# Performance work log

Hardware: AMD Instinct MI355X
Metric: run time of the kernel (lower is better)

The kernel has to match this reference:

```python
import jax, jax.numpy as jnp
import numpy as np

EMBED_DIM = 64  # scale factor dim (matches head dim)


def setup_inputs() -> dict:
    key0 = jax.random.key(0)
    kq, kk, kv = jax.random.split(key0, 3)
    shape = (2, 16, 2048, 64)  # [B, H, S, D]
    return {
        "query": jax.random.normal(kq, shape, dtype=jnp.float32),
        "key": jax.random.normal(kk, shape, dtype=jnp.float32),
        "value": jax.random.normal(kv, shape, dtype=jnp.float32),
    }


def reference(query, key, value):
    # qk = Q K^T / sqrt(embed_dim); softmax over last dim; @ V
    inv_scale = jnp.sqrt(jnp.asarray(EMBED_DIM, dtype=query.dtype))
    scores = jnp.einsum("bhqd,bhkd->bhqk", query, key) / inv_scale
    probs = jax.nn.softmax(scores, axis=-1)
    # dropout_p=0.0 -> identity (eval semantics)
    return jnp.einsum("bhqk,bhkd->bhqd", probs, value)
```

## Files before the change

kernel.cpp:

```cpp
#include <hip/hip_runtime.h>
#include <hip/hip_bf16.h>

#define S_LEN 2048
#define DDIM  64
#define NT    (S_LEN / 64)
#define SCALE  0.125f
#define SCALE2 0.18033688f
#define NELEM  4194304
#define NQROW  65536
#define WC_LGKM0 0xc07f

#if __has_builtin(__builtin_amdgcn_permlane32_swap) && __has_builtin(__builtin_amdgcn_permlane16_swap)
#define HAVE_PLSWAP 1
#else
#define HAVE_PLSWAP 0
#endif

typedef __attribute__((ext_vector_type(8))) short short8;
typedef __attribute__((ext_vector_type(4))) float floatx4;

__device__ __forceinline__ short f2bf(float f) {
    union { float f; unsigned u; } v; v.f = f;
    return (short)((v.u + 0x7fffu + ((v.u >> 16) & 1u)) >> 16);
}

__device__ __forceinline__ unsigned pk2bf(float a, float b) {
    unsigned r;
    asm("v_cvt_pk_bf16_f32 %0, %1, %2" : "=v"(r) : "v"(a), "v"(b));
    return r;
}

__device__ __forceinline__ float fexp2(float x) {
#if __has_builtin(__builtin_amdgcn_exp2f)
    return __builtin_amdgcn_exp2f(x);
#else
    return exp2f(x);
#endif
}

#if HAVE_PLSWAP
__device__ __forceinline__ void plswap32(unsigned &a, unsigned &b) {
    auto r = __builtin_amdgcn_permlane32_swap((int)a, (int)b, false, false);
    a = (unsigned)r[0]; b = (unsigned)r[1];
}
__device__ __forceinline__ void plswap16(unsigned &a, unsigned &b) {
    auto r = __builtin_amdgcn_permlane16_swap((int)a, (int)b, false, false);
    a = (unsigned)r[0]; b = (unsigned)r[1];
}
#endif

__global__ __launch_bounds__(256) void prep_kv(const float* __restrict__ K,
                                               const float* __restrict__ V,
                                               short* __restrict__ Kb,
                                               short* __restrict__ Vt) {
    const int bh = blockIdx.x & 31;
    const int st = blockIdx.x >> 5;
    const int t  = threadIdx.x;
    const size_t tile_off = (size_t)bh * (S_LEN * DDIM) + (size_t)st * (64 * DDIM);

    {
        const float* src = K + tile_off + t * 16;
        short* dst = Kb + tile_off + t * 16;
        #pragma unroll
        for (int h = 0; h < 2; ++h) {
            float4 a = *(const float4*)(src + h * 8);
            float4 b = *(const float4*)(src + h * 8 + 4);
            uint4 o;
            o.x = pk2bf(a.x, a.y); o.y = pk2bf(a.z, a.w);
            o.z = pk2bf(b.x, b.y); o.w = pk2bf(b.z, b.w);
            *(uint4*)(dst + h * 8) = o;
        }
    }

    {
        const int s4 = (t & 15) * 4;
        const int d4 = (t >> 4) * 4;
        const float* src = V + tile_off;
        float4 v0 = *(const float4*)(src + (size_t)(s4 + 0) * 64 + d4);
        float4 v1 = *(const float4*)(src + (size_t)(s4 + 1) * 64 + d4);
        float4 v2 = *(const float4*)(src + (size_t)(s4 + 2) * 64 + d4);
        float4 v3 = *(const float4*)(src + (size_t)(s4 + 3) * 64 + d4);
        const float* r0 = (const float*)&v0;
        const float* r1 = (const float*)&v1;
        const float* r2 = (const float*)&v2;
        const float* r3 = (const float*)&v3;
        short* dstb = Vt + (size_t)bh * (DDIM * S_LEN) + (size_t)st * 64 + s4;
        #pragma unroll
        for (int dd = 0; dd < 4; ++dd) {
            uint2 o;
            o.x = pk2bf(r0[dd], r1[dd]);
            o.y = pk2bf(r2[dd], r3[dd]);
            *(uint2*)(dstb + (size_t)(d4 + dd) * S_LEN) = o;
        }
    }
}

__global__ __launch_bounds__(512) void attn_sm8(
    const float* __restrict__ Q, const short* __restrict__ Kb,
    const short* __restrict__ Vt, float* __restrict__ O)
{
    __shared__ short Ks[2][2][64 * 64];
    __shared__ short Vs[2][2][64 * 64];
    __shared__ float Dl[128];
#if !HAVE_PLSWAP
    __shared__ short Pl[8][32 * 64];
#endif

    constexpr int NIT = NT / 2;

    const int tid  = threadIdx.x;
    const int wave = tid >> 6;
    const int grp  = wave >> 2;
    const int w4   = wave & 3;
    const int lane = tid & 63;
    const int l16  = lane & 15;
    const int quad = lane >> 4;
    const int x7   = l16 & 7;

    const int bh = blockIdx.x & 31;
    const int qt = blockIdx.x >> 5;
    const int ks = grp;
    const size_t base = (size_t)bh * (S_LEN * DDIM);

    const int g   = tid & 255;
    const int ci0 = g,        r0 = ci0 >> 3, c0 = (ci0 & 7) ^ (r0 & 7);
    const int ci1 = 256 + g,  r1 = ci1 >> 3, c1 = (ci1 & 7) ^ (r1 & 7);
    const size_t koff = (size_t)ks * NIT * (64 * 64);
    const size_t voff = (size_t)ks * NIT * 64;
    const short* pK0 = Kb + base + koff + r0 * 64 + c0 * 8;
    const short* pK1 = Kb + base + koff + r1 * 64 + c1 * 8;
    const short* pV0 = Vt + base + voff + (size_t)r0 * S_LEN + c0 * 8;
    const short* pV1 = Vt + base + voff + (size_t)r1 * S_LEN + c1 * 8;

    short8 rk0 = *(const short8*)pK0;
    short8 rk1 = *(const short8*)pK1;
    short8 rv0 = *(const short8*)pV0;
    short8 rv1 = *(const short8*)pV1;

    short8 qf[2][2];
    #pragma unroll
    for (int nq = 0; nq < 2; ++nq) {
        const float* qp = Q + base + (size_t)(qt * 128 + w4 * 32 + nq * 16 + l16) * 64 + quad * 8;
        #pragma unroll
        for (int kt = 0; kt < 2; ++kt) {
            float4 a = *(const float4*)(qp + kt * 32);
            float4 b = *(const float4*)(qp + kt * 32 + 4);
            union { unsigned u[4]; short8 s; } qc;
            qc.u[0] = pk2bf(a.x * SCALE2, a.y * SCALE2);
            qc.u[1] = pk2bf(a.z * SCALE2, a.w * SCALE2);
            qc.u[2] = pk2bf(b.x * SCALE2, b.y * SCALE2);
            qc.u[3] = pk2bf(b.z * SCALE2, b.w * SCALE2);
            qf[nq][kt] = qc.s;
        }
    }

    floatx4 oacc[2][4];
    float rs[2];
    #pragma unroll
    for (int mt = 0; mt < 2; ++mt) {
        #pragma unroll
        for (int dt = 0; dt < 4; ++dt) oacc[mt][dt] = (floatx4){0.f,0.f,0.f,0.f};
        rs[mt] = 0.f;
    }

    short* Ksg0 = &Ks[grp][0][0];
    short* Ksg1 = &Ks[grp][1][0];
    short* Vsg0 = &Vs[grp][0][0];
    short* Vsg1 = &Vs[grp][1][0];
#if !HAVE_PLSWAP
    short* Pw = &Pl[wave][0];
#endif

    *(short8*)&Ksg0[ci0 * 8] = rk0;
    *(short8*)&Ksg0[ci1 * 8] = rk1;
    *(short8*)&Vsg0[ci0 * 8] = rv0;
    *(short8*)&Vsg0[ci1 * 8] = rv1;
    {
        const int ok = 64 * 64, ov = 64;
        rk0 = *(const short8*)(pK0 + ok);
        rk1 = *(const short8*)(pK1 + ok);
        rv0 = *(const short8*)(pV0 + ov);
        rv1 = *(const short8*)(pV1 + ov);
    }
    __builtin_amdgcn_s_waitcnt(WC_LGKM0);
    __builtin_amdgcn_s_barrier();

    for (int kb = 0; kb < NIT; ++kb) {
        short* Ksc = (kb & 1) ? Ksg1 : Ksg0;
        short* Vsc = (kb & 1) ? Vsg1 : Vsg0;
        short* Ksn = (kb & 1) ? Ksg0 : Ksg1;
        short* Vsn = (kb & 1) ? Vsg0 : Vsg1;

        if (kb + 1 < NIT) {
            *(short8*)&Ksn[ci0 * 8] = rk0;
            *(short8*)&Ksn[ci1 * 8] = rk1;
            *(short8*)&Vsn[ci0 * 8] = rv0;
            *(short8*)&Vsn[ci1 * 8] = rv1;
            if (kb + 2 < NIT) {
                const int ok = (kb + 2) * (64 * 64), ov = (kb + 2) * 64;
                rk0 = *(const short8*)(pK0 + ok);
                rk1 = *(const short8*)(pK1 + ok);
                rv0 = *(const short8*)(pV0 + ov);
                rv1 = *(const short8*)(pV1 + ov);
            }
        }

        floatx4 sc[2][4];
        __builtin_amdgcn_s_setprio(1);
        #pragma unroll
        for (int mk = 0; mk < 4; ++mk) {
            floatx4 a0 = (floatx4){0.f,0.f,0.f,0.f};
            floatx4 a1 = (floatx4){0.f,0.f,0.f,0.f};
            #pragma unroll
            for (int kt = 0; kt < 2; ++kt) {
                const int csw = (kt * 4 + quad) ^ x7;
                short8 kf = *(const short8*)&Ksc[(mk * 16 + l16) * 64 + csw * 8];
                a0 = __builtin_amdgcn_mfma_f32_16x16x32_bf16(kf, qf[0][kt], a0, 0, 0, 0);
                a1 = __builtin_amdgcn_mfma_f32_16x16x32_bf16(kf, qf[1][kt], a1, 0, 0, 0);
            }
            sc[0][mk] = a0; sc[1][mk] = a1;
        }
        __builtin_amdgcn_s_setprio(0);

#if HAVE_PLSWAP
        unsigned pa[2][4], pb[2][4];
        #pragma unroll
        for (int nq = 0; nq < 2; ++nq) {
            #pragma unroll
            for (int mk = 0; mk < 4; ++mk) {
                float p0 = fexp2(sc[nq][mk][0]);
                float p1 = fexp2(sc[nq][mk][1]);
                float p2 = fexp2(sc[nq][mk][2]);
                float p3 = fexp2(sc[nq][mk][3]);
                rs[nq] += (p0 + p1) + (p2 + p3);
                pa[nq][mk] = pk2bf(p0, p1);
                pb[nq][mk] = pk2bf(p2, p3);
            }
        }

        #pragma unroll
        for (int kt = 0; kt < 2; ++kt) {
            short8 pf[2];
            #pragma unroll
            for (int nq = 0; nq < 2; ++nq) {
                unsigned a0 = pa[nq][2 * kt], a1 = pa[nq][2 * kt + 1];
                unsigned b0 = pb[nq][2 * kt], b1 = pb[nq][2 * kt + 1];
                plswap32(a0, a1); plswap16(a0, a1);
                plswap32(b0, b1); plswap16(b0, b1);
                union { unsigned u[4]; short8 s; } c;
                c.u[0] = a0; c.u[1] = b0; c.u[2] = a1; c.u[3] = b1;
                pf[nq] = c.s;
            }
            const int csw = (kt * 4 + quad) ^ x7;
            __builtin_amdgcn_s_setprio(1);
            #pragma unroll
            for (int dt = 0; dt < 4; ++dt) {
                short8 vf = *(const short8*)&Vsc[(dt * 16 + l16) * 64 + csw * 8];
                oacc[0][dt] = __builtin_amdgcn_mfma_f32_16x16x32_bf16(pf[0], vf, oacc[0][dt], 0, 0, 0);
                oacc[1][dt] = __builtin_amdgcn_mfma_f32_16x16x32_bf16(pf[1], vf, oacc[1][dt], 0, 0, 0);
            }
            __builtin_amdgcn_s_setprio(0);
        }
#else
        #pragma unroll
        for (int nq = 0; nq < 2; ++nq) {
            const int prow = (nq * 16 + l16) * 64;
            #pragma unroll
            for (int mk = 0; mk < 4; ++mk) {
                float p0 = fexp2(sc[nq][mk][0]);
                float p1 = fexp2(sc[nq][mk][1]);
                float p2 = fexp2(sc[nq][mk][2]);
                float p3 = fexp2(sc[nq][mk][3]);
                rs[nq] += (p0 + p1) + (p2 + p3);
                uint2 pv; pv.x = pk2bf(p0, p1); pv.y = pk2bf(p2, p3);
                const int c8 = (mk * 4 + quad) ^ (2 * x7);
                *(uint2*)&Pw[prow + c8 * 4] = pv;
            }
        }
        #pragma unroll
        for (int kt = 0; kt < 2; ++kt) {
            const int csw = (kt * 4 + quad) ^ x7;
            short8 pf0 = *(const short8*)&Pw[(l16)      * 64 + csw * 8];
            short8 pf1 = *(const short8*)&Pw[(16 + l16) * 64 + csw * 8];
            #pragma unroll
            for (int dt = 0; dt < 4; ++dt) {
                short8 vf = *(const short8*)&Vsc[(dt * 16 + l16) * 64 + csw * 8];
                oacc[0][dt] = __builtin_amdgcn_mfma_f32_16x16x32_bf16(pf0, vf, oacc[0][dt], 0, 0, 0);
                oacc[1][dt] = __builtin_amdgcn_mfma_f32_16x16x32_bf16(pf1, vf, oacc[1][dt], 0, 0, 0);
            }
        }
#endif

        __builtin_amdgcn_s_waitcnt(WC_LGKM0);
        __builtin_amdgcn_s_barrier();
    }

    float sred[2];
    #pragma unroll
    for (int nq = 0; nq < 2; ++nq) {
        float s = rs[nq];
        s += __shfl_xor(s, 16, 64);
        s += __shfl_xor(s, 32, 64);
        sred[nq] = s;
    }

    if (quad == 0) {
        if (grp == 1) Dl[w4 * 32 + l16]      = sred[0];
        else          Dl[w4 * 32 + 16 + l16] = sred[1];
    }

    {
        float* NbMine = (float*)&Ks[grp][0][0];
        const int pmt = 1 - grp;
        #pragma unroll
        for (int dt = 0; dt < 4; ++dt)
            #pragma unroll
            for (int r = 0; r < 4; ++r)
                NbMine[(dt * 4 + r) * 256 + w4 * 64 + lane] = oacc[pmt][dt][r];
    }
    __syncthreads();

    {
        const float* NbOther = (const float*)&Ks[1 - grp][0][0];
        const int cmt = grp;
        const float dother = Dl[w4 * 32 + (grp ? 16 : 0) + l16];
        const float invc = 1.0f / (sred[cmt] + dother);
        #pragma unroll
        for (int r = 0; r < 4; ++r) {
            const int row = qt * 128 + w4 * 32 + cmt * 16 + quad * 4 + r;
            const float it = __shfl(invc, quad * 4 + r, 64);
            float* op = O + base + (size_t)row * 64 + l16;
            #pragma unroll
            for (int dt = 0; dt < 4; ++dt)
                op[dt * 16] = (oacc[cmt][dt][r] + NbOther[(dt * 4 + r) * 256 + w4 * 64 + lane]) * it;
        }
    }
}

#define BQ    64
#define BKEY  64
#define KPAD  72

__global__ __launch_bounds__(256) void attn_kernel(
    const float* __restrict__ Q, const float* __restrict__ K,
    const float* __restrict__ V, float* __restrict__ O)
{
    __shared__ short Ksh[BKEY * KPAD];
    __shared__ short Vtt[DDIM * KPAD];
    __shared__ short Pls[4][16 * KPAD];

    const int tid  = threadIdx.x;
    const int wave = tid >> 6;
    const int lane = tid & 63;
    const int l16  = lane & 15;
    const int quad = lane >> 4;

    const int bh = blockIdx.x & 31;
    const int qt = blockIdx.x >> 5;
    const size_t base = (size_t)bh * S_LEN * DDIM;

    const int qrow = qt * BQ + wave * 16 + l16;
    short8 qf[2];
    {
        const float* qp = Q + base + (size_t)qrow * DDIM + quad * 8;
        #pragma unroll
        for (int kt = 0; kt < 2; ++kt) {
            float4 a = *(const float4*)(qp + kt * 32);
            float4 b = *(const float4*)(qp + kt * 32 + 4);
            short* d = (short*)&qf[kt];
            d[0]=f2bf(a.x*SCALE); d[1]=f2bf(a.y*SCALE); d[2]=f2bf(a.z*SCALE); d[3]=f2bf(a.w*SCALE);
            d[4]=f2bf(b.x*SCALE); d[5]=f2bf(b.y*SCALE); d[6]=f2bf(b.z*SCALE); d[7]=f2bf(b.w*SCALE);
        }
    }

    float m_i[4], l_i[4];
    floatx4 oacc[4];
    #pragma unroll
    for (int r = 0; r < 4; ++r) { m_i[r] = -3.0e38f; l_i[r] = 0.f; }
    #pragma unroll
    for (int dt = 0; dt < 4; ++dt) oacc[dt] = (floatx4){0.f, 0.f, 0.f, 0.f};

    const int skey = tid >> 2;
    const int scol = (tid & 3) * 4;

    for (int kb = 0; kb < S_LEN / BKEY; ++kb) {
        const float* Kg = K + base + (size_t)kb * BKEY * DDIM + (size_t)skey * DDIM;
        const float* Vg = V + base + (size_t)kb * BKEY * DDIM + (size_t)skey * DDIM;
        #pragma unroll
        for (int i = 0; i < 4; ++i) {
            const int c = scol + i * 16;
            float4 kv = *(const float4*)(Kg + c);
            short* kd = &Ksh[skey * KPAD + c];
            kd[0]=f2bf(kv.x); kd[1]=f2bf(kv.y); kd[2]=f2bf(kv.z); kd[3]=f2bf(kv.w);
            float4 vv = *(const float4*)(Vg + c);
            Vtt[(c+0)*KPAD + skey] = f2bf(vv.x);
            Vtt[(c+1)*KPAD + skey] = f2bf(vv.y);
            Vtt[(c+2)*KPAD + skey] = f2bf(vv.z);
            Vtt[(c+3)*KPAD + skey] = f2bf(vv.w);
        }
        __syncthreads();

        floatx4 sc[4];
        #pragma unroll
        for (int nt = 0; nt < 4; ++nt) {
            floatx4 acc = (floatx4){0.f, 0.f, 0.f, 0.f};
            #pragma unroll
            for (int kt = 0; kt < 2; ++kt) {
                short8 kf = *(const short8*)&Ksh[(nt*16 + l16) * KPAD + kt*32 + quad*8];
                acc = __builtin_amdgcn_mfma_f32_16x16x32_bf16(qf[kt], kf, acc, 0, 0, 0);
            }
            sc[nt] = acc;
        }

        short* Pw = &Pls[wave][0];
        #pragma unroll
        for (int r = 0; r < 4; ++r) {
            float mx = fmaxf(fmaxf(sc[0][r], sc[1][r]), fmaxf(sc[2][r], sc[3][r]));
            #pragma unroll
            for (int off = 1; off < 16; off <<= 1)
                mx = fmaxf(mx, __shfl_xor(mx, off, 64));
            const float mnew  = fmaxf(m_i[r], mx);
            const float alpha = __expf(m_i[r] - mnew);
            m_i[r] = mnew;
            float rsum = 0.f;
            #pragma unroll
            for (int nt = 0; nt < 4; ++nt) {
                float p = __expf(sc[nt][r] - mnew);
                rsum += p;
                Pw[(quad*4 + r) * KPAD + nt*16 + l16] = f2bf(p);
            }
            #pragma unroll
            for (int off = 1; off < 16; off <<= 1)
                rsum += __shfl_xor(rsum, off, 64);
            l_i[r] = l_i[r] * alpha + rsum;
            oacc[0][r] *= alpha; oacc[1][r] *= alpha;
            oacc[2][r] *= alpha; oacc[3][r] *= alpha;
        }

        #pragma unroll
        for (int kt = 0; kt < 2; ++kt) {
            short8 pf = *(const short8*)&Pw[l16 * KPAD + kt*32 + quad*8];
            #pragma unroll
            for (int dt = 0; dt < 4; ++dt) {
                short8 vf = *(const short8*)&Vtt[(dt*16 + l16) * KPAD + kt*32 + quad*8];
                oacc[dt] = __builtin_amdgcn_mfma_f32_16x16x32_bf16(pf, vf, oacc[dt], 0, 0, 0);
            }
        }
        __syncthreads();
    }

    #pragma unroll
    for (int r = 0; r < 4; ++r) {
        const float inv = 1.0f / l_i[r];
        const int row = qt * BQ + wave * 16 + quad * 4 + r;
        float* op = O + base + (size_t)row * DDIM + l16;
        #pragma unroll
        for (int dt = 0; dt < 4; ++dt)
            op[dt * 16] = oacc[dt][r] * inv;
    }
}

extern "C" void kernel_launch(void* const* d_in, const int* in_sizes, int n_in,
                              void* d_out, int out_size, void* d_ws, size_t ws_size,
                              hipStream_t stream) {
    const float* Q = (const float*)d_in[0];
    const float* K = (const float*)d_in[1];
    const float* V = (const float*)d_in[2];
    float* O = (float*)d_out;

    const size_t prep_bytes = (size_t)NELEM * 2 * 2;

    if (ws_size >= prep_bytes) {
        short* Kb  = (short*)d_ws;
        short* Vtp = (short*)d_ws + NELEM;
        prep_kv<<<dim3(1024), dim3(256), 0, stream>>>(K, V, Kb, Vtp);
        attn_sm8<<<dim3(512), dim3(512), 0, stream>>>(Q, Kb, Vtp, O);
    } else {
        attn_kernel<<<dim3(1024), dim3(256), 0, stream>>>(Q, K, V, O);
    }
}
```

Before: 153.0 us.

## Software-pipeline QK^T one tile ahead of softmax/PV in attention main loop

Restructures the main loop so the QK^T scores for tile kb are computed while the softmax and PV for tile kb-1 run, using two score register sets and a macro-unrolled loop with prologue and epilogue. The V shared-memory buffer now lags K by one stage, and K and V global prefetch distances differ. It also swaps the inline-asm bf16 pack for integer rounding arithmetic and adds a min-blocks launch bound, which constrains registers. Holding extra live score registers risks spills under the tighter register budget, and the software bf16 conversion costs extra VALU instructions.

```diff
diff --git a/kernel.cpp b/kernel.cpp
--- a/kernel.cpp
+++ b/kernel.cpp
@@ -10,12 +10,6 @@
 #define NQROW  65536
 #define WC_LGKM0 0xc07f
 
-#if __has_builtin(__builtin_amdgcn_permlane32_swap) && __has_builtin(__builtin_amdgcn_permlane16_swap)
-#define HAVE_PLSWAP 1
-#else
-#define HAVE_PLSWAP 0
-#endif
-
 typedef __attribute__((ext_vector_type(8))) short short8;
 typedef __attribute__((ext_vector_type(4))) float floatx4;
 
@@ -25,9 +19,10 @@
 }
 
 __device__ __forceinline__ unsigned pk2bf(float a, float b) {
-    unsigned r;
-    asm("v_cvt_pk_bf16_f32 %0, %1, %2" : "=v"(r) : "v"(a), "v"(b));
-    return r;
+    union { float f; unsigned u; } x, y; x.f = a; y.f = b;
+    unsigned lo = (x.u + 0x7fffu + ((x.u >> 16) & 1u)) >> 16;
+    unsigned hi = (y.u + 0x7fffu + ((y.u >> 16) & 1u)) & 0xffff0000u;
+    return lo | hi;
 }
 
 __device__ __forceinline__ float fexp2(float x) {
@@ -38,7 +33,6 @@
 #endif
 }
 
-#if HAVE_PLSWAP
 __device__ __forceinline__ void plswap32(unsigned &a, unsigned &b) {
     auto r = __builtin_amdgcn_permlane32_swap((int)a, (int)b, false, false);
     a = (unsigned)r[0]; b = (unsigned)r[1];
@@ -47,7 +41,6 @@
     auto r = __builtin_amdgcn_permlane16_swap((int)a, (int)b, false, false);
     a = (unsigned)r[0]; b = (unsigned)r[1];
 }
-#endif
 
 __global__ __launch_bounds__(256) void prep_kv(const float* __restrict__ K,
                                                const float* __restrict__ V,
@@ -95,16 +88,99 @@
     }
 }
 
-__global__ __launch_bounds__(512) void attn_sm8(
+#define TILE_BODY(KB, P, SCC, SCP, DO_QK, DO_SM, DO_BAR) do {                      \
+    const int kb_ = (KB);                                                          \
+    if (kb_ + 1 < NIT) {                            \
+        short* Kn_ = (P) ? Ksg0 : Ksg1;                                            \
+        *(short8*)&Kn_[ci0 * 8] = rk0;                                             \
+        *(short8*)&Kn_[ci1 * 8] = rk1;                                             \
+    }                                                                              \
+    if (kb_ < NIT) {                                    \
+        short* Vn_ = (P) ? Vsg1 : Vsg0;                                            \
+        *(short8*)&Vn_[ci0 * 8] = rv0;                                             \
+        *(short8*)&Vn_[ci1 * 8] = rv1;                                             \
+    }                                                                              \
+    if (kb_ + 2 < NIT) {                                     \
+        const int ok_ = (kb_ + 2) * (64 * 64);                                     \
+        rk0 = *(const short8*)(pK0 + ok_);                                         \
+        rk1 = *(const short8*)(pK1 + ok_);                                         \
+    }                                                                              \
+    if (kb_ + 1 < NIT) {                                     \
+        const int ov_ = (kb_ + 1) * 64;                                            \
+        rv0 = *(const short8*)(pV0 + ov_);                                         \
+        rv1 = *(const short8*)(pV1 + ov_);                                         \
+    }                                                                              \
+    if (DO_QK) {                                         \
+        short* Kc_ = (P) ? Ksg1 : Ksg0;                                            \
+        __builtin_amdgcn_s_setprio(1);                                             \
+        _Pragma("unroll")                                                          \
+        for (int mk = 0; mk < 4; ++mk) {                                           \
+            floatx4 a0_ = (floatx4){0.f, 0.f, 0.f, 0.f};                           \
+            floatx4 a1_ = (floatx4){0.f, 0.f, 0.f, 0.f};                           \
+            _Pragma("unroll")                                                      \
+            for (int kt = 0; kt < 2; ++kt) {                                       \
+                const int csw_ = (kt * 4 + quad) ^ x7;                             \
+                short8 kf_ = *(const short8*)&Kc_[(mk * 16 + l16) * 64 + csw_ * 8];\
+                a0_ = __builtin_amdgcn_mfma_f32_16x16x32_bf16(kf_, qf[0][kt], a0_, 0, 0, 0); \
+                a1_ = __builtin_amdgcn_mfma_f32_16x16x32_bf16(kf_, qf[1][kt], a1_, 0, 0, 0); \
+            }                                                                      \
+            SCC[0][mk] = a0_; SCC[1][mk] = a1_;                                    \
+        }                                                                          \
+        __builtin_amdgcn_s_setprio(0);                                             \
+    }                                                                              \
+    if (DO_SM) {                                      \
+        unsigned pa_[2][4], pb_[2][4];                                             \
+        _Pragma("unroll")                                                          \
+        for (int nq = 0; nq < 2; ++nq) {                                           \
+            _Pragma("unroll")                                                      \
+            for (int mk = 0; mk < 4; ++mk) {                                       \
+                float p0_ = fexp2(SCP[nq][mk][0]);                                 \
+                float p1_ = fexp2(SCP[nq][mk][1]);                                 \
+                float p2_ = fexp2(SCP[nq][mk][2]);                                 \
+                float p3_ = fexp2(SCP[nq][mk][3]);                                 \
+                rs[nq] += (p0_ + p1_) + (p2_ + p3_);                               \
+                pa_[nq][mk] = pk2bf(p0_, p1_);                                     \
+                pb_[nq][mk] = pk2bf(p2_, p3_);                                     \
+            }                                                                      \
+        }                                                                          \
+        short* Vc_ = (P) ? Vsg0 : Vsg1;                \
+        _Pragma("unroll")                                                          \
+        for (int kt = 0; kt < 2; ++kt) {                                           \
+            short8 pf_[2];                                                         \
+            _Pragma("unroll")                                                      \
+            for (int nq = 0; nq < 2; ++nq) {                                       \
+                unsigned a0_ = pa_[nq][2 * kt], a1_ = pa_[nq][2 * kt + 1];         \
+                unsigned b0_ = pb_[nq][2 * kt], b1_ = pb_[nq][2 * kt + 1];         \
+                plswap32(a0_, a1_); plswap16(a0_, a1_);                            \
+                plswap32(b0_, b1_); plswap16(b0_, b1_);                            \
+                union { unsigned u[4]; short8 s; } c_;                             \
+                c_.u[0] = a0_; c_.u[1] = b0_; c_.u[2] = a1_; c_.u[3] = b1_;        \
+                pf_[nq] = c_.s;                                                    \
+            }                                                                      \
+            const int csw_ = (kt * 4 + quad) ^ x7;                                 \
+            __builtin_amdgcn_s_setprio(1);                                         \
+            _Pragma("unroll")                                                      \
+            for (int dt = 0; dt < 4; ++dt) {                                       \
+                short8 vf_ = *(const short8*)&Vc_[(dt * 16 + l16) * 64 + csw_ * 8];\
+                oacc[0][dt] = __builtin_amdgcn_mfma_f32_16x16x32_bf16(pf_[0], vf_, oacc[0][dt], 0, 0, 0); \
+                oacc[1][dt] = __builtin_amdgcn_mfma_f32_16x16x32_bf16(pf_[1], vf_, oacc[1][dt], 0, 0, 0); \
+            }                                                                      \
+            __builtin_amdgcn_s_setprio(0);                                         \
+        }                                                                          \
+    }                                                                              \
+    if (DO_BAR) {                                                                  \
+        __builtin_amdgcn_s_waitcnt(WC_LGKM0);                                      \
+        __builtin_amdgcn_s_barrier();                                              \
+    }                                                                              \
+} while (0)
+
+__global__ __launch_bounds__(512, 4) void attn_sm8(
     const float* __restrict__ Q, const short* __restrict__ Kb,
     const short* __restrict__ Vt, float* __restrict__ O)
 {
     __shared__ short Ks[2][2][64 * 64];
     __shared__ short Vs[2][2][64 * 64];
     __shared__ float Dl[128];
-#if !HAVE_PLSWAP
-    __shared__ short Pl[8][32 * 64];
-#endif
 
     constexpr int NIT = NT / 2;
 
@@ -132,10 +208,10 @@
     const short* pV0 = Vt + base + voff + (size_t)r0 * S_LEN + c0 * 8;
     const short* pV1 = Vt + base + voff + (size_t)r1 * S_LEN + c1 * 8;
 
-    short8 rk0 = *(const short8*)pK0;
-    short8 rk1 = *(const short8*)pK1;
-    short8 rv0 = *(const short8*)pV0;
-    short8 rv1 = *(const short8*)pV1;
+    short* Ksg0 = &Ks[grp][0][0];
+    short* Ksg1 = &Ks[grp][1][0];
+    short* Vsg0 = &Vs[grp][0][0];
+    short* Vsg1 = &Vs[grp][1][0];
 
     short8 qf[2][2];
     #pragma unroll
@@ -159,141 +235,31 @@
     #pragma unroll
     for (int mt = 0; mt < 2; ++mt) {
         #pragma unroll
-        for (int dt = 0; dt < 4; ++dt) oacc[mt][dt] = (floatx4){0.f,0.f,0.f,0.f};
+        for (int dt = 0; dt < 4; ++dt) oacc[mt][dt] = (floatx4){0.f, 0.f, 0.f, 0.f};
         rs[mt] = 0.f;
     }
 
-    short* Ksg0 = &Ks[grp][0][0];
-    short* Ksg1 = &Ks[grp][1][0];
-    short* Vsg0 = &Vs[grp][0][0];
-    short* Vsg1 = &Vs[grp][1][0];
-#if !HAVE_PLSWAP
-    short* Pw = &Pl[wave][0];
-#endif
-
+    floatx4 scA[2][4], scB[2][4];
+
+    short8 rk0 = *(const short8*)pK0;
+    short8 rk1 = *(const short8*)pK1;
     *(short8*)&Ksg0[ci0 * 8] = rk0;
     *(short8*)&Ksg0[ci1 * 8] = rk1;
-    *(short8*)&Vsg0[ci0 * 8] = rv0;
-    *(short8*)&Vsg0[ci1 * 8] = rv1;
-    {
-        const int ok = 64 * 64, ov = 64;
-        rk0 = *(const short8*)(pK0 + ok);
-        rk1 = *(const short8*)(pK1 + ok);
-        rv0 = *(const short8*)(pV0 + ov);
-        rv1 = *(const short8*)(pV1 + ov);
-    }
+    rk0 = *(const short8*)(pK0 + 64 * 64);
+    rk1 = *(const short8*)(pK1 + 64 * 64);
+    short8 rv0 = *(const short8*)pV0;
+    short8 rv1 = *(const short8*)pV1;
     __builtin_amdgcn_s_waitcnt(WC_LGKM0);
     __builtin_amdgcn_s_barrier();
 
-    for (int kb = 0; kb < NIT; ++kb) {
-        short* Ksc = (kb & 1) ? Ksg1 : Ksg0;
-        short* Vsc = (kb & 1) ? Vsg1 : Vsg0;
-        short* Ksn = (kb & 1) ? Ksg0 : Ksg1;
-        short* Vsn = (kb & 1) ? Vsg0 : Vsg1;
-
-        if (kb + 1 < NIT) {
-            *(short8*)&Ksn[ci0 * 8] = rk0;
-            *(short8*)&Ksn[ci1 * 8] = rk1;
-            *(short8*)&Vsn[ci0 * 8] = rv0;
-            *(short8*)&Vsn[ci1 * 8] = rv1;
-            if (kb + 2 < NIT) {
-                const int ok = (kb + 2) * (64 * 64), ov = (kb + 2) * 64;
-                rk0 = *(const short8*)(pK0 + ok);
-                rk1 = *(const short8*)(pK1 + ok);
-                rv0 = *(const short8*)(pV0 + ov);
-                rv1 = *(const short8*)(pV1 + ov);
-            }
-        }
-
-        floatx4 sc[2][4];
-        __builtin_amdgcn_s_setprio(1);
-        #pragma unroll
-        for (int mk = 0; mk < 4; ++mk) {
-            floatx4 a0 = (floatx4){0.f,0.f,0.f,0.f};
-            floatx4 a1 = (floatx4){0.f,0.f,0.f,0.f};
-            #pragma unroll
-            for (int kt = 0; kt < 2; ++kt) {
-                const int csw = (kt * 4 + quad) ^ x7;
-                short8 kf = *(const short8*)&Ksc[(mk * 16 + l16) * 64 + csw * 8];
-                a0 = __builtin_amdgcn_mfma_f32_16x16x32_bf16(kf, qf[0][kt], a0, 0, 0, 0);
-                a1 = __builtin_amdgcn_mfma_f32_16x16x32_bf16(kf, qf[1][kt], a1, 0, 0, 0);
-            }
-            sc[0][mk] = a0; sc[1][mk] = a1;
-        }
-        __builtin_amdgcn_s_setprio(0);
-
-#if HAVE_PLSWAP
-        unsigned pa[2][4], pb[2][4];
-        #pragma unroll
-        for (int nq = 0; nq < 2; ++nq) {
-            #pragma unroll
-            for (int mk = 0; mk < 4; ++mk) {
-                float p0 = fexp2(sc[nq][mk][0]);
-                float p1 = fexp2(sc[nq][mk][1]);
-                float p2 = fexp2(sc[nq][mk][2]);
-                float p3 = fexp2(sc[nq][mk][3]);
-                rs[nq] += (p0 + p1) + (p2 + p3);
-                pa[nq][mk] = pk2bf(p0, p1);
-                pb[nq][mk] = pk2bf(p2, p3);
-            }
-        }
-
-        #pragma unroll
-        for (int kt = 0; kt < 2; ++kt) {
-            short8 pf[2];
-            #pragma unroll
-            for (int nq = 0; nq < 2; ++nq) {
-                unsigned a0 = pa[nq][2 * kt], a1 = pa[nq][2 * kt + 1];
-                unsigned b0 = pb[nq][2 * kt], b1 = pb[nq][2 * kt + 1];
-                plswap32(a0, a1); plswap16(a0, a1);
-                plswap32(b0, b1); plswap16(b0, b1);
-                union { unsigned u[4]; short8 s; } c;
-                c.u[0] = a0; c.u[1] = b0; c.u[2] = a1; c.u[3] = b1;
-                pf[nq] = c.s;
-            }
-            const int csw = (kt * 4 + quad) ^ x7;
-            __builtin_amdgcn_s_setprio(1);
-            #pragma unroll
-            for (int dt = 0; dt < 4; ++dt) {
-                short8 vf = *(const short8*)&Vsc[(dt * 16 + l16) * 64 + csw * 8];
-                oacc[0][dt] = __builtin_amdgcn_mfma_f32_16x16x32_bf16(pf[0], vf, oacc[0][dt], 0, 0, 0);
-                oacc[1][dt] = __builtin_amdgcn_mfma_f32_16x16x32_bf16(pf[1], vf, oacc[1][dt], 0, 0, 0);
-            }
-            __builtin_amdgcn_s_setprio(0);
-        }
-#else
-        #pragma unroll
-        for (int nq = 0; nq < 2; ++nq) {
-            const int prow = (nq * 16 + l16) * 64;
-            #pragma unroll
-            for (int mk = 0; mk < 4; ++mk) {
-                float p0 = fexp2(sc[nq][mk][0]);
-                float p1 = fexp2(sc[nq][mk][1]);
-                float p2 = fexp2(sc[nq][mk][2]);
-                float p3 = fexp2(sc[nq][mk][3]);
-                rs[nq] += (p0 + p1) + (p2 + p3);
-                uint2 pv; pv.x = pk2bf(p0, p1); pv.y = pk2bf(p2, p3);
-                const int c8 = (mk * 4 + quad) ^ (2 * x7);
-                *(uint2*)&Pw[prow + c8 * 4] = pv;
-            }
-        }
-        #pragma unroll
-        for (int kt = 0; kt < 2; ++kt) {
-            const int csw = (kt * 4 + quad) ^ x7;
-            short8 pf0 = *(const short8*)&Pw[(l16)      * 64 + csw * 8];
-            short8 pf1 = *(const short8*)&Pw[(16 + l16) * 64 + csw * 8];
-            #pragma unroll
-            for (int dt = 0; dt < 4; ++dt) {
-                short8 vf = *(const short8*)&Vsc[(dt * 16 + l16) * 64 + csw * 8];
-                oacc[0][dt] = __builtin_amdgcn_mfma_f32_16x16x32_bf16(pf0, vf, oacc[0][dt], 0, 0, 0);
-                oacc[1][dt] = __builtin_amdgcn_mfma_f32_16x16x32_bf16(pf1, vf, oacc[1][dt], 0, 0, 0);
-            }
-        }
-#endif
-
-        __builtin_amdgcn_s_waitcnt(WC_LGKM0);
-        __builtin_amdgcn_s_barrier();
-    }
+    TILE_BODY(0, 0, scA, scB, true, false, true);
+    for (int k2 = 0; k2 < 7; ++k2) {
+        const int kb = 1 + 2 * k2;
+        TILE_BODY(kb,     1, scB, scA, true, true, true);
+        TILE_BODY(kb + 1, 0, scA, scB, true, true, true);
+    }
+    TILE_BODY(15, 1, scB, scA, true, true, true);
+    TILE_BODY(16, 0, scA, scB, false, true, false);
 
     float sred[2];
     #pragma unroll
```

After: 330.6 us. 2.16x slower.
